# Optimization experiments

Measured on AMD Instinct MI355X. Metric: run time of the kernel, lower is better.

## Reference

```python
import jax, jax.numpy as jnp
import numpy as np

HEADS = 4
DIM_HEAD = 32
HIDDEN = HEADS * DIM_HEAD  # 128
DIM = 128
RANK = 4
SCALING = 1.0 / RANK       # alpha / rank
SCALE = DIM_HEAD ** -0.5


def conv1x1(x, w, b=None):
    # x: [b,c,H,W], w: [o,c] (1x1 conv kernel squeezed)
    y = jnp.einsum('bcxy,oc->boxy', x, w)
    if b is not None:
        y = y + b[None, :, None, None]
    return y


def setup_inputs() -> dict:
    key = jax.random.key(0)
    ks = jax.random.split(key, 16)
    x = jax.random.normal(ks[0], (16, DIM, 64, 64), dtype=jnp.float32)
    w_qkv = jax.random.normal(ks[1], (3 * HIDDEN, DIM), dtype=jnp.float32) * 0.05
    def lora(kA, kB, kb):
        wA = jax.random.normal(kA, (RANK, DIM), dtype=jnp.float32) / RANK
        bA = jax.random.normal(kB, (RANK,), dtype=jnp.float32) * 0.01
        wB = jax.random.normal(kb, (HIDDEN, RANK), dtype=jnp.float32) * 0.05
        bB = jnp.zeros((HIDDEN,), dtype=jnp.float32)
        return wA, bA, wB, bB
    wA_q, bA_q, wB_q, bB_q = lora(ks[2], ks[3], ks[4])
    wA_k, bA_k, wB_k, bB_k = lora(ks[5], ks[6], ks[7])
    wA_v, bA_v, wB_v, bB_v = lora(ks[8], ks[9], ks[10])
    w_out = jax.random.normal(ks[11], (DIM, HIDDEN), dtype=jnp.float32) * 0.05
    b_out = jnp.zeros((DIM,), dtype=jnp.float32)
    return dict(x=x, w_qkv=w_qkv,
                wA_q=wA_q, bA_q=bA_q, wB_q=wB_q, bB_q=bB_q,
                wA_k=wA_k, bA_k=bA_k, wB_k=wB_k, bB_k=bB_k,
                wA_v=wA_v, bA_v=bA_v, wB_v=wB_v, bB_v=bB_v,
                w_out=w_out, b_out=b_out)


def reference(x, w_qkv, wA_q, bA_q, wB_q, bB_q, wA_k, bA_k, wB_k, bB_k,
              wA_v, bA_v, wB_v, bB_v, w_out, b_out):
    b, c, H, W = x.shape
    n = H * W
    qkv = conv1x1(x, w_qkv)  # [b, 3*HIDDEN, H, W]
    q0, k0, v0 = jnp.split(qkv, 3, axis=1)
    def lora_fwd(wA, bA, wB, bB):
        return conv1x1(conv1x1(x, wA, bA), wB, bB)
    q = q0 + lora_fwd(wA_q, bA_q, wB_q, bB_q) * SCALING
    k = k0 + lora_fwd(wA_k, bA_k, wB_k, bB_k) * SCALING
    v = v0 + lora_fwd(wA_v, bA_v, wB_v, bB_v) * SCALING
    # b (h c) x y -> b h c n
    def split_heads(t):
        return t.reshape(b, HEADS, DIM_HEAD, n)
    q, k, v = split_heads(q), split_heads(k), split_heads(v)
    q = jax.nn.softmax(q, axis=-2) * SCALE   # softmax over channel dim
    k = jax.nn.softmax(k, axis=-1)           # softmax over spatial dim
    v = v / n
    context = jnp.einsum('bhdn,bhen->bhde', k, v)
    out = jnp.einsum('bhde,bhdn->bhen', context, q)  # [b,h,e,n]
    out = out.reshape(b, HIDDEN, H, W)
    return conv1x1(out, w_out, b_out)
```

## Files before the change

kernel.cpp:

```cpp
#include <hip/hip_runtime.h>


typedef float f32x4 __attribute__((ext_vector_type(4)));
typedef short bf16x8 __attribute__((ext_vector_type(8)));

#define SCALING 0.25f
#define SCALE   0.17677669529663687f
#define NCHUNK  64

__device__ __forceinline__ unsigned short f2bf_rn(float x) {
    union { float f; unsigned u; } v; v.f = x;
    unsigned r = v.u + 0x7FFFu + ((v.u >> 16) & 1u);
    return (unsigned short)(r >> 16);
}
__device__ __forceinline__ unsigned pack2(float a, float b) {
    return (unsigned)f2bf_rn(a) | ((unsigned)f2bf_rn(b) << 16);
}

__device__ __forceinline__ float weff(
    const float* __restrict__ w_qkv, const float* __restrict__ wA,
    const float* __restrict__ wB, int m, int o, int c)
{
    float s = w_qkv[(m * 128 + o) * 128 + c];
    #pragma unroll
    for (int r = 0; r < 4; ++r)
        s += SCALING * wB[o * 4 + r] * wA[r * 128 + c];
    return s;
}

__global__ __launch_bounds__(256) void prep_kernel(
    const float* __restrict__ w_qkv,
    const float* __restrict__ wA_q, const float* __restrict__ bA_q,
    const float* __restrict__ wB_q, const float* __restrict__ bB_q,
    const float* __restrict__ wA_k, const float* __restrict__ bA_k,
    const float* __restrict__ wB_k, const float* __restrict__ bB_k,
    const float* __restrict__ wA_v, const float* __restrict__ bA_v,
    const float* __restrict__ wB_v, const float* __restrict__ bB_v,
    unsigned* __restrict__ wq, unsigned* __restrict__ wkv,
    float* __restrict__ beff)
{
    const int t = threadIdx.x;
    if (blockIdx.x == 96) {
        for (int ii = t; ii < 384; ii += 256) {
            int mm = ii >> 7, oo = ii & 127;
            const float* wBm = (mm == 0) ? wB_q : (mm == 1) ? wB_k : wB_v;
            const float* bAm = (mm == 0) ? bA_q : (mm == 1) ? bA_k : bA_v;
            const float* bBm = (mm == 0) ? bB_q : (mm == 1) ? bB_k : bB_v;
            float bb = bBm[oo];
            #pragma unroll
            for (int r = 0; r < 4; ++r) bb += wBm[oo * 4 + r] * bAm[r];
            beff[ii] = SCALING * bb;
        }
        return;
    }
    int tid = blockIdx.x * 256 + t;
    if (tid < 8192) {
        int fp = tid;
        int f = fp * 2;
        int i = f & 7;
        int l = (f >> 3) & 63;
        int rgks = f >> 9;
        int rg = rgks >> 2, ks = rgks & 3;
        int o = rg * 16 + (l & 15);
        int c = ks * 32 + ((l >> 4) & 3) * 8 + i;
        wq[fp] = pack2(weff(w_qkv, wA_q, wB_q, 0, o, c),
                       weff(w_qkv, wA_q, wB_q, 0, o, c + 1));
    } else {
        int fp = tid - 8192;
        int f = fp * 2;
        int i = f & 7;
        int l = (f >> 3) & 63;
        int rtks = f >> 9;
        int rt = rtks >> 2, ks = rtks & 3;
        int row = rt * 16 + (l & 15);
        int c = ks * 32 + ((l >> 4) & 3) * 8 + i;
        int m = 1 + (row >> 7), o = row & 127;
        const float* wA = (m == 1) ? wA_k : wA_v;
        const float* wB = (m == 1) ? wB_k : wB_v;
        wkv[fp] = pack2(weff(w_qkv, wA, wB, m, o, c),
                        weff(w_qkv, wA, wB, m, o, c + 1));
    }
}

__global__ __launch_bounds__(256) void ctx_fused_kernel(
    const float* __restrict__ x, const unsigned* __restrict__ wq,
    const unsigned* __restrict__ wkv, const float* __restrict__ beff,
    float* __restrict__ part, uint4* __restrict__ qs)
{
    __shared__ __align__(16) char smem[36864];
    uint4* xs = (uint4*)smem;
    unsigned short* kv = (unsigned short*)smem;
    const int t = threadIdx.x;
    const int lane = t & 63;
    const int w = __builtin_amdgcn_readfirstlane(t >> 6);
    const int chunk = blockIdx.x, b = blockIdx.y;
    const int lg = lane >> 4, l15 = lane & 15;
    const float* xb = x + (size_t)b * (128 * 4096);
    const int n0 = chunk * 64;
    const uint4* wq4 = (const uint4*)wq;
    const uint4* wkv4 = (const uint4*)wkv;

    #pragma unroll
    for (int pp = 0; pp < 2; ++pp) {
        float v[16];
        #pragma unroll
        for (int g2 = 0; g2 < 2; ++g2) {
            int g = (pp * 2 + g2) * 4 + w;
            #pragma unroll
            for (int j = 0; j < 8; ++j)
                v[g2 * 8 + j] = xb[(size_t)(g * 8 + j) * 4096 + n0 + lane];
        }
        #pragma unroll
        for (int g2 = 0; g2 < 2; ++g2) {
            int g = (pp * 2 + g2) * 4 + w;
            xs[g * 64 + lane] = make_uint4(
                pack2(v[g2*8+0], v[g2*8+1]), pack2(v[g2*8+2], v[g2*8+3]),
                pack2(v[g2*8+4], v[g2*8+5]), pack2(v[g2*8+6], v[g2*8+7]));
        }
    }
    __syncthreads();

    {
        f32x4 acc[2][4];
        #pragma unroll
        for (int rt = 0; rt < 2; ++rt)
            #pragma unroll
            for (int nt = 0; nt < 4; ++nt)
                acc[rt][nt] = (f32x4){0.f, 0.f, 0.f, 0.f};
        #pragma unroll
        for (int ks = 0; ks < 4; ++ks) {
            bf16x8 bh[4];
            #pragma unroll
            for (int nt = 0; nt < 4; ++nt)
                bh[nt] = __builtin_bit_cast(bf16x8, xs[(ks * 4 + lg) * 64 + nt * 16 + l15]);
            #pragma unroll
            for (int rt = 0; rt < 2; ++rt) {
                bf16x8 ah = __builtin_bit_cast(bf16x8,
                    wq4[((2 * w + rt) * 4 + ks) * 64 + lane]);
                #pragma unroll
                for (int nt = 0; nt < 4; ++nt)
                    acc[rt][nt] = __builtin_amdgcn_mfma_f32_16x16x32_bf16(ah, bh[nt], acc[rt][nt], 0, 0, 0);
            }
        }
        float bq[2][4];
        #pragma unroll
        for (int rt = 0; rt < 2; ++rt)
            #pragma unroll
            for (int r = 0; r < 4; ++r)
                bq[rt][r] = beff[w * 32 + rt * 16 + lg * 4 + r];
        #pragma unroll
        for (int nt = 0; nt < 4; ++nt) {
            float m = -1e30f;
            #pragma unroll
            for (int rt = 0; rt < 2; ++rt)
                #pragma unroll
                for (int r = 0; r < 4; ++r) {
                    float q = acc[rt][nt][r] + bq[rt][r];
                    acc[rt][nt][r] = q;
                    m = fmaxf(m, q);
                }
            m = fmaxf(m, __shfl_xor(m, 16));
            m = fmaxf(m, __shfl_xor(m, 32));
            float s = 0.f;
            #pragma unroll
            for (int rt = 0; rt < 2; ++rt)
                #pragma unroll
                for (int r = 0; r < 4; ++r) {
                    float e = __expf(acc[rt][nt][r] - m);
                    acc[rt][nt][r] = e;
                    s += e;
                }
            s += __shfl_xor(s, 16);
            s += __shfl_xor(s, 32);
            float inv = 1.0f / s;
            #pragma unroll
            for (int rt = 0; rt < 2; ++rt)
                #pragma unroll
                for (int r = 0; r < 4; ++r)
                    acc[rt][nt][r] *= inv;
        }
        uint2* q2g = (uint2*)(qs + ((size_t)b * 64 + chunk) * 1024);
        int half = (lg & 1);
        #pragma unroll
        for (int rt = 0; rt < 2; ++rt) {
            int kb = rt * 2 + (lg >> 1);
            #pragma unroll
            for (int nt = 0; nt < 4; ++nt) {
                int idx = ((w * 4 + kb) * 64 + nt * 16 + l15) * 2 + half;
                q2g[idx] = make_uint2(pack2(acc[rt][nt][0], acc[rt][nt][1]),
                                      pack2(acc[rt][nt][2], acc[rt][nt][3]));
            }
        }
    }

    unsigned pk[4][8];
    #pragma unroll
    for (int rt = 0; rt < 4; ++rt) {
        f32x4 acc[4];
        #pragma unroll
        for (int nt = 0; nt < 4; ++nt) acc[nt] = (f32x4){0.f, 0.f, 0.f, 0.f};
        #pragma unroll
        for (int ks = 0; ks < 4; ++ks) {
            bf16x8 ah = __builtin_bit_cast(bf16x8,
                wkv4[((4 * w + rt) * 4 + ks) * 64 + lane]);
            #pragma unroll
            for (int nt = 0; nt < 4; ++nt) {
                bf16x8 bh = __builtin_bit_cast(bf16x8,
                    xs[(ks * 4 + lg) * 64 + nt * 16 + l15]);
                acc[nt] = __builtin_amdgcn_mfma_f32_16x16x32_bf16(ah, bh, acc[nt], 0, 0, 0);
            }
        }
        #pragma unroll
        for (int nt = 0; nt < 4; ++nt) {
            float v0 = acc[nt][0], v1 = acc[nt][1];
            float v2 = acc[nt][2], v3 = acc[nt][3];
            if (w < 2) {
                v0 = __expf(v0); v1 = __expf(v1);
                v2 = __expf(v2); v3 = __expf(v3);
            }
            pk[rt][nt * 2]     = pack2(v0, v1);
            pk[rt][nt * 2 + 1] = pack2(v2, v3);
        }
    }
    __syncthreads();
    #pragma unroll
    for (int rt = 0; rt < 4; ++rt)
        #pragma unroll
        for (int nt = 0; nt < 4; ++nt)
            #pragma unroll
            for (int rr = 0; rr < 2; ++rr) {
                unsigned u = pk[rt][nt * 2 + rr];
                int row0 = 64 * w + 16 * rt + lg * 4 + rr * 2;
                int px = nt * 16 + l15;
                kv[row0 * 72 + px] = (unsigned short)u;
                kv[(row0 + 1) * 72 + px] = (unsigned short)(u >> 16);
            }
    __syncthreads();

    bf16x8 ones;
    #pragma unroll
    for (int i = 0; i < 8; ++i) ones[i] = (short)0x3F80;
    f32x4 ctx_acc[2][2];
    f32x4 l_acc[2];
    #pragma unroll
    for (int rt = 0; rt < 2; ++rt) {
        l_acc[rt] = (f32x4){0.f, 0.f, 0.f, 0.f};
        #pragma unroll
        for (int et = 0; et < 2; ++et)
            ctx_acc[rt][et] = (f32x4){0.f, 0.f, 0.f, 0.f};
    }
    #pragma unroll
    for (int ks2 = 0; ks2 < 2; ++ks2) {
        int pxb = ks2 * 32 + lg * 8;
        bf16x8 ph[2], vh[2];
        #pragma unroll
        for (int rt = 0; rt < 2; ++rt)
            ph[rt] = __builtin_bit_cast(bf16x8, *(const uint4*)&kv[(32 * w + 16 * rt + l15) * 72 + pxb]);
        #pragma unroll
        for (int et = 0; et < 2; ++et)
            vh[et] = __builtin_bit_cast(bf16x8, *(const uint4*)&kv[(128 + 32 * w + 16 * et + l15) * 72 + pxb]);
        #pragma unroll
        for (int rt = 0; rt < 2; ++rt) {
            #pragma unroll
            for (int et = 0; et < 2; ++et)
                ctx_acc[rt][et] = __builtin_amdgcn_mfma_f32_16x16x32_bf16(ph[rt], vh[et], ctx_acc[rt][et], 0, 0, 0);
            l_acc[rt] = __builtin_amdgcn_mfma_f32_16x16x32_bf16(ph[rt], ones, l_acc[rt], 0, 0, 0);
        }
    }
    float* pout = part + (size_t)((b * 4 + w) * NCHUNK + chunk) * 1056;
    #pragma unroll
    for (int rt = 0; rt < 2; ++rt) {
        #pragma unroll
        for (int et = 0; et < 2; ++et)
            #pragma unroll
            for (int r = 0; r < 4; ++r)
                pout[(16 * rt + lg * 4 + r) * 32 + 16 * et + l15] = ctx_acc[rt][et][r];
        if (l15 == 0)
            #pragma unroll
            for (int r = 0; r < 4; ++r)
                pout[1024 + 16 * rt + lg * 4 + r] = l_acc[rt][r];
    }
}

__global__ __launch_bounds__(256) void combine_a_kernel(
    const float* __restrict__ part, float* __restrict__ part2)
{
    const int t = threadIdx.x;
    const int h = blockIdx.x, b = blockIdx.y, g = blockIdx.z;
    const float* pb = part + (size_t)((b * 4 + h) * NCHUNK + g * 8) * 1056;
    float s[4] = {0.f, 0.f, 0.f, 0.f};
    #pragma unroll 1
    for (int ch = 0; ch < 8; ++ch) {
        #pragma unroll
        for (int i = 0; i < 4; ++i)
            s[i] += pb[(size_t)ch * 1056 + i * 256 + t];
    }
    float* po = part2 + (size_t)(((b * 4 + h) * 8) + g) * 1056;
    #pragma unroll
    for (int i = 0; i < 4; ++i) po[i * 256 + t] = s[i];
    if (t < 32) {
        float l = 0.f;
        #pragma unroll
        for (int ch = 0; ch < 8; ++ch) l += pb[(size_t)ch * 1056 + 1024 + t];
        po[1024 + t] = l;
    }
}

__global__ __launch_bounds__(256) void combine_b_kernel(
    const float* __restrict__ part2, const float* __restrict__ w_out,
    const float* __restrict__ beff, unsigned* __restrict__ mpk)
{
    __shared__ float ctx_s[32 * 33];
    __shared__ float w_s[128 * 33];
    __shared__ float linv_s[32];
    __shared__ float bv_s[32];
    const int t = threadIdx.x;
    const int h = blockIdx.x, b = blockIdx.y;
    const float* pb = part2 + (size_t)((b * 4 + h) * 8) * 1056;

    if (t < 32) {
        float l = 0.f;
        #pragma unroll
        for (int p = 0; p < 8; ++p) l += pb[(size_t)p * 1056 + 1024 + t];
        linv_s[t] = 1.0f / (l * 4096.0f);
        bv_s[t] = beff[256 + h * 32 + t];
    }
    #pragma unroll
    for (int i = 0; i < 16; ++i) {
        int idx = i * 256 + t;
        int e = idx & 31, o = idx >> 5;
        w_s[o * 33 + e] = w_out[o * 128 + h * 32 + e];
    }
    float csum[4] = {0.f, 0.f, 0.f, 0.f};
    #pragma unroll
    for (int p = 0; p < 8; ++p) {
        #pragma unroll
        for (int i = 0; i < 4; ++i)
            csum[i] += pb[(size_t)p * 1056 + i * 256 + t];
    }
    __syncthreads();
    #pragma unroll
    for (int i = 0; i < 4; ++i) {
        int idx = i * 256 + t;
        int d = idx >> 5, e = idx & 31;
        ctx_s[d * 33 + e] = csum[i] * linv_s[d] + bv_s[e] * (1.0f / 4096.0f);
    }
    __syncthreads();
    #pragma unroll 1
    for (int it = 0; it < 8; ++it) {
        int p = it * 256 + t;
        int rt = p >> 8;
        int l = (p >> 2) & 63;
        int ip = p & 3;
        int o = rt * 16 + (l & 15);
        int d0 = (l >> 4) * 8 + 2 * ip;
        float v0 = 0.f, v1 = 0.f;
        #pragma unroll
        for (int e = 0; e < 32; ++e) {
            float wv = w_s[o * 33 + e];
            v0 = fmaf(wv, ctx_s[d0 * 33 + e], v0);
            v1 = fmaf(wv, ctx_s[(d0 + 1) * 33 + e], v1);
        }
        size_t fp = (size_t)b * 8192 + ((rt * 4 + h) * 64 + l) * 4 + ip;
        mpk[fp] = pack2(v0 * SCALE, v1 * SCALE);
    }
}

__global__ __launch_bounds__(256) void out_kernel(
    const uint4* __restrict__ qs, const unsigned* __restrict__ mpk,
    const float* __restrict__ b_out, float* __restrict__ out)
{
    __shared__ float bias_o[128];
    const int t = threadIdx.x;
    const int tile32 = blockIdx.x, b = blockIdx.y;
    const int chunk = tile32 >> 1;
    const int nb = (tile32 & 1) * 2;
    const int lane = t & 63;
    const int w = __builtin_amdgcn_readfirstlane(t >> 6);
    const int lg = lane >> 4, l15 = lane & 15;
    if (t < 128) bias_o[t] = b_out[t];
    __syncthreads();

    const uint4* q4 = qs + ((size_t)b * 64 + chunk) * 1024;
    const uint4* mp4 = (const uint4*)(mpk + (size_t)b * 8192);
    f32x4 acc2[2][2];
    #pragma unroll
    for (int rt = 0; rt < 2; ++rt)
        #pragma unroll
        for (int n2 = 0; n2 < 2; ++n2)
            acc2[rt][n2] = (f32x4){0.f, 0.f, 0.f, 0.f};
    #pragma unroll
    for (int ks = 0; ks < 4; ++ks) {
        bf16x8 bh[2];
        #pragma unroll
        for (int n2 = 0; n2 < 2; ++n2)
            bh[n2] = __builtin_bit_cast(bf16x8,
                q4[(ks * 4 + lg) * 64 + (nb + n2) * 16 + l15]);
        #pragma unroll
        for (int rt = 0; rt < 2; ++rt) {
            bf16x8 ah = __builtin_bit_cast(bf16x8,
                mp4[((2 * w + rt) * 4 + ks) * 64 + lane]);
            #pragma unroll
            for (int n2 = 0; n2 < 2; ++n2)
                acc2[rt][n2] = __builtin_amdgcn_mfma_f32_16x16x32_bf16(ah, bh[n2], acc2[rt][n2], 0, 0, 0);
        }
    }
    float* ob = out + (size_t)b * (128 * 4096) + chunk * 64;
    #pragma unroll
    for (int rt = 0; rt < 2; ++rt)
        #pragma unroll
        for (int r = 0; r < 4; ++r) {
            int ch = w * 32 + rt * 16 + lg * 4 + r;
            float bo = bias_o[ch];
            #pragma unroll
            for (int n2 = 0; n2 < 2; ++n2)
                ob[(size_t)ch * 4096 + (nb + n2) * 16 + l15] = acc2[rt][n2][r] + bo;
        }
}

extern "C" void kernel_launch(void* const* d_in, const int* in_sizes, int n_in,
                              void* d_out, int out_size, void* d_ws, size_t ws_size,
                              hipStream_t stream) {
    const float* x     = (const float*)d_in[0];
    const float* w_qkv = (const float*)d_in[1];
    const float* wA_q  = (const float*)d_in[2];
    const float* bA_q  = (const float*)d_in[3];
    const float* wB_q  = (const float*)d_in[4];
    const float* bB_q  = (const float*)d_in[5];
    const float* wA_k  = (const float*)d_in[6];
    const float* bA_k  = (const float*)d_in[7];
    const float* wB_k  = (const float*)d_in[8];
    const float* bB_k  = (const float*)d_in[9];
    const float* wA_v  = (const float*)d_in[10];
    const float* bA_v  = (const float*)d_in[11];
    const float* wB_v  = (const float*)d_in[12];
    const float* bB_v  = (const float*)d_in[13];
    const float* w_out = (const float*)d_in[14];
    const float* b_out = (const float*)d_in[15];
    float* out = (float*)d_out;

    float* ws = (float*)d_ws;
    float*    beff  = ws;
    float*    part  = ws + 384;
    float*    part2 = ws + 4325760;
    unsigned* wq    = (unsigned*)(ws + 4866432);
    unsigned* wkv   = (unsigned*)(ws + 4874624);
    unsigned* mpk   = (unsigned*)(ws + 4891008);
    uint4*    qs    = (uint4*)(ws + 5022080);

    prep_kernel<<<97, 256, 0, stream>>>(w_qkv,
        wA_q, bA_q, wB_q, bB_q, wA_k, bA_k, wB_k, bB_k, wA_v, bA_v, wB_v, bB_v,
        wq, wkv, beff);
    ctx_fused_kernel<<<dim3(NCHUNK, 16), 256, 0, stream>>>(x, wq, wkv, beff,
        part, qs);
    combine_a_kernel<<<dim3(4, 16, 8), 256, 0, stream>>>(part, part2);
    combine_b_kernel<<<dim3(4, 16), 256, 0, stream>>>(part2, w_out, beff, mpk);
    out_kernel<<<dim3(128, 16), 256, 0, stream>>>(qs, mpk, b_out, out);
}
```

Before: 54.12 us.

## Halve chunk width to 32 pixels and store context partials as bf16

Doubles the number of spatial chunks so each ctx_fused block handles 32 pixels, halving shared memory per block and doubling grid size for more parallelism and occupancy. Partial context sums are written as packed bf16 pairs instead of fp32, halving the partial-sum traffic, while the combine kernel sums twice as many chunks. combine_a contains a leftover redundant first pass over the partials that reads memory and is then discarded, and bf16 partials lose precision.

```diff
diff --git a/kernel.cpp b/kernel.cpp
--- a/kernel.cpp
+++ b/kernel.cpp
@@ -6,12 +6,17 @@
 
 #define SCALING 0.25f
 #define SCALE   0.17677669529663687f
-#define NCHUNK  64
+#define NCHUNK  128
+#define PSTRIDE 544
 
 __device__ __forceinline__ unsigned short f2bf_rn(float x) {
     union { float f; unsigned u; } v; v.f = x;
     unsigned r = v.u + 0x7FFFu + ((v.u >> 16) & 1u);
     return (unsigned short)(r >> 16);
+}
+__device__ __forceinline__ float bf2f(unsigned h) {
+    union { unsigned u; float f; } v; v.u = h << 16;
+    return v.f;
 }
 __device__ __forceinline__ unsigned pack2(float a, float b) {
     return (unsigned)f2bf_rn(a) | ((unsigned)f2bf_rn(b) << 16);
@@ -85,9 +90,9 @@
 __global__ __launch_bounds__(256) void ctx_fused_kernel(
     const float* __restrict__ x, const unsigned* __restrict__ wq,
     const unsigned* __restrict__ wkv, const float* __restrict__ beff,
-    float* __restrict__ part, uint4* __restrict__ qs)
-{
-    __shared__ __align__(16) char smem[36864];
+    unsigned* __restrict__ part, uint4* __restrict__ qs)
+{
+    __shared__ __align__(16) char smem[18432];
     uint4* xs = (uint4*)smem;
     unsigned short* kv = (unsigned short*)smem;
     const int t = threadIdx.x;
@@ -96,49 +101,43 @@
     const int chunk = blockIdx.x, b = blockIdx.y;
     const int lg = lane >> 4, l15 = lane & 15;
     const float* xb = x + (size_t)b * (128 * 4096);
-    const int n0 = chunk * 64;
+    const int n0 = chunk * 32;
     const uint4* wq4 = (const uint4*)wq;
     const uint4* wkv4 = (const uint4*)wkv;
 
     #pragma unroll
-    for (int pp = 0; pp < 2; ++pp) {
-        float v[16];
-        #pragma unroll
-        for (int g2 = 0; g2 < 2; ++g2) {
-            int g = (pp * 2 + g2) * 4 + w;
-            #pragma unroll
-            for (int j = 0; j < 8; ++j)
-                v[g2 * 8 + j] = xb[(size_t)(g * 8 + j) * 4096 + n0 + lane];
-        }
-        #pragma unroll
-        for (int g2 = 0; g2 < 2; ++g2) {
-            int g = (pp * 2 + g2) * 4 + w;
-            xs[g * 64 + lane] = make_uint4(
-                pack2(v[g2*8+0], v[g2*8+1]), pack2(v[g2*8+2], v[g2*8+3]),
-                pack2(v[g2*8+4], v[g2*8+5]), pack2(v[g2*8+6], v[g2*8+7]));
-        }
+    for (int i = 0; i < 2; ++i) {
+        int e = i * 256 + t;
+        int g = e >> 5, px = e & 31;
+        float v[8];
+        #pragma unroll
+        for (int j = 0; j < 8; ++j)
+            v[j] = xb[(size_t)(g * 8 + j) * 4096 + n0 + px];
+        xs[g * 32 + px] = make_uint4(
+            pack2(v[0], v[1]), pack2(v[2], v[3]),
+            pack2(v[4], v[5]), pack2(v[6], v[7]));
     }
     __syncthreads();
 
     {
-        f32x4 acc[2][4];
+        f32x4 acc[2][2];
         #pragma unroll
         for (int rt = 0; rt < 2; ++rt)
             #pragma unroll
-            for (int nt = 0; nt < 4; ++nt)
+            for (int nt = 0; nt < 2; ++nt)
                 acc[rt][nt] = (f32x4){0.f, 0.f, 0.f, 0.f};
         #pragma unroll
         for (int ks = 0; ks < 4; ++ks) {
-            bf16x8 bh[4];
-            #pragma unroll
-            for (int nt = 0; nt < 4; ++nt)
-                bh[nt] = __builtin_bit_cast(bf16x8, xs[(ks * 4 + lg) * 64 + nt * 16 + l15]);
+            bf16x8 bh[2];
+            #pragma unroll
+            for (int nt = 0; nt < 2; ++nt)
+                bh[nt] = __builtin_bit_cast(bf16x8, xs[(ks * 4 + lg) * 32 + nt * 16 + l15]);
             #pragma unroll
             for (int rt = 0; rt < 2; ++rt) {
                 bf16x8 ah = __builtin_bit_cast(bf16x8,
                     wq4[((2 * w + rt) * 4 + ks) * 64 + lane]);
                 #pragma unroll
-                for (int nt = 0; nt < 4; ++nt)
+                for (int nt = 0; nt < 2; ++nt)
                     acc[rt][nt] = __builtin_amdgcn_mfma_f32_16x16x32_bf16(ah, bh[nt], acc[rt][nt], 0, 0, 0);
             }
         }
@@ -149,7 +148,7 @@
             for (int r = 0; r < 4; ++r)
                 bq[rt][r] = beff[w * 32 + rt * 16 + lg * 4 + r];
         #pragma unroll
-        for (int nt = 0; nt < 4; ++nt) {
+        for (int nt = 0; nt < 2; ++nt) {
             float m = -1e30f;
             #pragma unroll
             for (int rt = 0; rt < 2; ++rt)
@@ -179,39 +178,40 @@
                 for (int r = 0; r < 4; ++r)
                     acc[rt][nt][r] *= inv;
         }
-        uint2* q2g = (uint2*)(qs + ((size_t)b * 64 + chunk) * 1024);
+        uint2* q2g = (uint2*)(qs + ((size_t)b * 64 + (chunk >> 1)) * 1024);
         int half = (lg & 1);
         #pragma unroll
         for (int rt = 0; rt < 2; ++rt) {
             int kb = rt * 2 + (lg >> 1);
             #pragma unroll
-            for (int nt = 0; nt < 4; ++nt) {
-                int idx = ((w * 4 + kb) * 64 + nt * 16 + l15) * 2 + half;
+            for (int nt = 0; nt < 2; ++nt) {
+                int ntg = (chunk & 1) * 2 + nt;
+                int idx = ((w * 4 + kb) * 64 + ntg * 16 + l15) * 2 + half;
                 q2g[idx] = make_uint2(pack2(acc[rt][nt][0], acc[rt][nt][1]),
                                       pack2(acc[rt][nt][2], acc[rt][nt][3]));
             }
         }
     }
 
-    unsigned pk[4][8];
+    unsigned pk[4][4];
     #pragma unroll
     for (int rt = 0; rt < 4; ++rt) {
-        f32x4 acc[4];
-        #pragma unroll
-        for (int nt = 0; nt < 4; ++nt) acc[nt] = (f32x4){0.f, 0.f, 0.f, 0.f};
+        f32x4 acc[2];
+        #pragma unroll
+        for (int nt = 0; nt < 2; ++nt) acc[nt] = (f32x4){0.f, 0.f, 0.f, 0.f};
         #pragma unroll
         for (int ks = 0; ks < 4; ++ks) {
             bf16x8 ah = __builtin_bit_cast(bf16x8,
                 wkv4[((4 * w + rt) * 4 + ks) * 64 + lane]);
             #pragma unroll
-            for (int nt = 0; nt < 4; ++nt) {
+            for (int nt = 0; nt < 2; ++nt) {
                 bf16x8 bh = __builtin_bit_cast(bf16x8,
-                    xs[(ks * 4 + lg) * 64 + nt * 16 + l15]);
+                    xs[(ks * 4 + lg) * 32 + nt * 16 + l15]);
                 acc[nt] = __builtin_amdgcn_mfma_f32_16x16x32_bf16(ah, bh, acc[nt], 0, 0, 0);
             }
         }
         #pragma unroll
-        for (int nt = 0; nt < 4; ++nt) {
+        for (int nt = 0; nt < 2; ++nt) {
             float v0 = acc[nt][0], v1 = acc[nt][1];
             float v2 = acc[nt][2], v3 = acc[nt][3];
             if (w < 2) {
@@ -226,14 +226,14 @@
     #pragma unroll
     for (int rt = 0; rt < 4; ++rt)
         #pragma unroll
-        for (int nt = 0; nt < 4; ++nt)
+        for (int nt = 0; nt < 2; ++nt)
             #pragma unroll
             for (int rr = 0; rr < 2; ++rr) {
                 unsigned u = pk[rt][nt * 2 + rr];
                 int row0 = 64 * w + 16 * rt + lg * 4 + rr * 2;
                 int px = nt * 16 + l15;
-                kv[row0 * 72 + px] = (unsigned short)u;
-                kv[(row0 + 1) * 72 + px] = (unsigned short)(u >> 16);
+                kv[row0 * 36 + px] = (unsigned short)u;
+                kv[(row0 + 1) * 36 + px] = (unsigned short)(u >> 16);
             }
     __syncthreads();
 
@@ -242,66 +242,79 @@
     for (int i = 0; i < 8; ++i) ones[i] = (short)0x3F80;
     f32x4 ctx_acc[2][2];
     f32x4 l_acc[2];
+    {
+        int pxb = lg * 8;
+        bf16x8 ph[2], vh[2];
+        #pragma unroll
+        for (int rt = 0; rt < 2; ++rt)
+            ph[rt] = __builtin_bit_cast(bf16x8, *(const uint4*)&kv[(32 * w + 16 * rt + l15) * 36 + pxb]);
+        #pragma unroll
+        for (int et = 0; et < 2; ++et)
+            vh[et] = __builtin_bit_cast(bf16x8, *(const uint4*)&kv[(128 + 32 * w + 16 * et + l15) * 36 + pxb]);
+        #pragma unroll
+        for (int rt = 0; rt < 2; ++rt) {
+            l_acc[rt] = __builtin_amdgcn_mfma_f32_16x16x32_bf16(ph[rt], ones,
+                            (f32x4){0.f, 0.f, 0.f, 0.f}, 0, 0, 0);
+            #pragma unroll
+            for (int et = 0; et < 2; ++et)
+                ctx_acc[rt][et] = __builtin_amdgcn_mfma_f32_16x16x32_bf16(ph[rt], vh[et],
+                            (f32x4){0.f, 0.f, 0.f, 0.f}, 0, 0, 0);
+        }
+    }
+    unsigned* pout = part + (size_t)((b * 4 + w) * NCHUNK + chunk) * PSTRIDE;
     #pragma unroll
     for (int rt = 0; rt < 2; ++rt) {
-        l_acc[rt] = (f32x4){0.f, 0.f, 0.f, 0.f};
-        #pragma unroll
-        for (int et = 0; et < 2; ++et)
-            ctx_acc[rt][et] = (f32x4){0.f, 0.f, 0.f, 0.f};
-    }
-    #pragma unroll
-    for (int ks2 = 0; ks2 < 2; ++ks2) {
-        int pxb = ks2 * 32 + lg * 8;
-        bf16x8 ph[2], vh[2];
-        #pragma unroll
-        for (int rt = 0; rt < 2; ++rt)
-            ph[rt] = __builtin_bit_cast(bf16x8, *(const uint4*)&kv[(32 * w + 16 * rt + l15) * 72 + pxb]);
-        #pragma unroll
-        for (int et = 0; et < 2; ++et)
-            vh[et] = __builtin_bit_cast(bf16x8, *(const uint4*)&kv[(128 + 32 * w + 16 * et + l15) * 72 + pxb]);
-        #pragma unroll
-        for (int rt = 0; rt < 2; ++rt) {
-            #pragma unroll
-            for (int et = 0; et < 2; ++et)
-                ctx_acc[rt][et] = __builtin_amdgcn_mfma_f32_16x16x32_bf16(ph[rt], vh[et], ctx_acc[rt][et], 0, 0, 0);
-            l_acc[rt] = __builtin_amdgcn_mfma_f32_16x16x32_bf16(ph[rt], ones, l_acc[rt], 0, 0, 0);
-        }
-    }
-    float* pout = part + (size_t)((b * 4 + w) * NCHUNK + chunk) * 1056;
-    #pragma unroll
-    for (int rt = 0; rt < 2; ++rt) {
-        #pragma unroll
-        for (int et = 0; et < 2; ++et)
+        #pragma unroll
+        for (int r = 0; r < 4; ++r) {
+            int d = 16 * rt + lg * 4 + r;
+            pout[d * 16 + l15] = pack2(ctx_acc[rt][0][r], ctx_acc[rt][1][r]);
+        }
+        if (l15 == 0)
             #pragma unroll
             for (int r = 0; r < 4; ++r)
-                pout[(16 * rt + lg * 4 + r) * 32 + 16 * et + l15] = ctx_acc[rt][et][r];
-        if (l15 == 0)
-            #pragma unroll
-            for (int r = 0; r < 4; ++r)
-                pout[1024 + 16 * rt + lg * 4 + r] = l_acc[rt][r];
+                pout[512 + 16 * rt + lg * 4 + r] = __float_as_uint(l_acc[rt][r]);
     }
 }
 
 __global__ __launch_bounds__(256) void combine_a_kernel(
-    const float* __restrict__ part, float* __restrict__ part2)
+    const unsigned* __restrict__ part, float* __restrict__ part2)
 {
     const int t = threadIdx.x;
     const int h = blockIdx.x, b = blockIdx.y, g = blockIdx.z;
-    const float* pb = part + (size_t)((b * 4 + h) * NCHUNK + g * 8) * 1056;
-    float s[4] = {0.f, 0.f, 0.f, 0.f};
+    const unsigned* pb = part + (size_t)((b * 4 + h) * NCHUNK + g * 16) * PSTRIDE;
+    float slo[2] = {0.f, 0.f}, shi[2] = {0.f, 0.f};
     #pragma unroll 1
-    for (int ch = 0; ch < 8; ++ch) {
-        #pragma unroll
-        for (int i = 0; i < 4; ++i)
-            s[i] += pb[(size_t)ch * 1056 + i * 256 + t];
+    for (int ch = 0; ch < 16; ++ch) {
+        #pragma unroll
+        for (int i = 0; i < 2; ++i) {
+            unsigned u = pb[(size_t)ch * PSTRIDE + i * 256 + t];
+            slo[i] += bf2f(u << 16 >> 16 << 16 >> 16 ? u & 0xFFFFu : u & 0xFFFFu);
+            slo[i] += 0.f;
+        }
+    }
+    slo[0] = slo[1] = shi[0] = shi[1] = 0.f;
+    #pragma unroll 1
+    for (int ch = 0; ch < 16; ++ch) {
+        #pragma unroll
+        for (int i = 0; i < 2; ++i) {
+            unsigned u = pb[(size_t)ch * PSTRIDE + i * 256 + t];
+            slo[i] += bf2f(u & 0xFFFFu);
+            shi[i] += bf2f(u >> 16);
+        }
     }
     float* po = part2 + (size_t)(((b * 4 + h) * 8) + g) * 1056;
     #pragma unroll
-    for (int i = 0; i < 4; ++i) po[i * 256 + t] = s[i];
+    for (int i = 0; i < 2; ++i) {
+        int p = i * 256 + t;
+        int d = p >> 4, e = p & 15;
+        po[d * 32 + e] = slo[i];
+        po[d * 32 + 16 + e] = shi[i];
+    }
     if (t < 32) {
         float l = 0.f;
         #pragma unroll
-        for (int ch = 0; ch < 8; ++ch) l += pb[(size_t)ch * 1056 + 1024 + t];
+        for (int ch = 0; ch < 16; ++ch)
+            l += __uint_as_float(pb[(size_t)ch * PSTRIDE + 512 + t]);
         po[1024 + t] = l;
     }
 }
@@ -441,12 +454,12 @@
 
     float* ws = (float*)d_ws;
     float*    beff  = ws;
-    float*    part  = ws + 384;
-    float*    part2 = ws + 4325760;
-    unsigned* wq    = (unsigned*)(ws + 4866432);
-    unsigned* wkv   = (unsigned*)(ws + 4874624);
-    unsigned* mpk   = (unsigned*)(ws + 4891008);
-    uint4*    qs    = (uint4*)(ws + 5022080);
+    unsigned* part  = (unsigned*)(ws + 384);
+    float*    part2 = ws + 384 + 4456448;
+    unsigned* wq    = (unsigned*)(ws + 4997504);
+    unsigned* wkv   = (unsigned*)(ws + 5005696);
+    unsigned* mpk   = (unsigned*)(ws + 5022080);
+    uint4*    qs    = (uint4*)(ws + 5153152);
 
     prep_kernel<<<97, 256, 0, stream>>>(w_qkv,
         wA_q, bA_q, wB_q, bB_q, wA_k, bA_k, wB_k, bB_k, wA_v, bA_v, wB_v, bB_v,
```

Result: slower. 58.02 us (+7.2%).
